# Kernel optimization log

Measured on AMD Instinct MI355X. Metric: run time of the kernel, lower is better.

Reference implementation:

```python
import jax, jax.numpy as jnp
import numpy as np


def setup_inputs() -> dict:
    key = jax.random.key(0)
    kq, kk, kv = jax.random.split(key, 3)
    shape = (4, 16, 2048, 128)  # [B, H, S, D]
    return {
        "query": jax.random.normal(kq, shape, dtype=jnp.float32),
        "key": jax.random.normal(kk, shape, dtype=jnp.float32),
        "value": jax.random.normal(kv, shape, dtype=jnp.float32),
    }


def reference(query, key, value):
    # NOTE: the original torch code computes math.sqrt(d) but immediately
    # overwrites it with d itself, so the scale is 1/D (not 1/sqrt(D)).
    d = query.shape[-1]
    score = jnp.einsum("bhqd,bhkd->bhqk", query, key) / d  # [B,H,S,S]
    attn = jax.nn.softmax(score, axis=-1)
    return jnp.einsum("bhqk,bhkd->bhqd", attn, value)
```

## Files before the change

### kernel.cpp

```cpp
#include <hip/hip_runtime.h>
#include <stdint.h>

typedef __bf16 bf16x8 __attribute__((ext_vector_type(8)));
typedef __bf16 bf16x2 __attribute__((ext_vector_type(2)));
typedef float  f32x4  __attribute__((ext_vector_type(4)));
typedef unsigned short u16x4 __attribute__((ext_vector_type(4)));
typedef unsigned short u16x8 __attribute__((ext_vector_type(8)));

#define DEVI __device__ __forceinline__

constexpr int Bc = 4, Hc = 16, Ss = 2048, Dd = 128;
constexpr int BH = Bc * Hc;
constexpr int BM = 256;
constexpr int MT = 4;
constexpr int BN = 32;
constexpr int NTIL = Ss / BN;
constexpr int LDP = 40;
constexpr float SCALE = 1.44269504088896340736f / 128.0f;

constexpr int TILE_B = BN * Dd * 2;
constexpr int SK_OFF = 0;
constexpr int SV_OFF = 2 * TILE_B;
constexpr int SP_OFF = 4 * TILE_B;
constexpr int LDS_BYTES = SP_OFF + BM * LDP * 2;
static_assert(LDS_BYTES == 53248, "mt=4 config");

DEVI unsigned short f2bf_bits(float x) {
  unsigned u = __builtin_bit_cast(unsigned, x);
  u += 0x7fffu + ((u >> 16) & 1u);
  return (unsigned short)(u >> 16);
}
DEVI __bf16 f2bf(float x) {
  unsigned short b = f2bf_bits(x);
  return __builtin_bit_cast(__bf16, b);
}

DEVI float exp2_hw(float x) { return __builtin_amdgcn_exp2f(x); }

DEVI void gload_lds16(const void* g, void* l) {
  __builtin_amdgcn_global_load_lds(
      (const __attribute__((address_space(1))) unsigned*)(uintptr_t)g,
      (__attribute__((address_space(3))) unsigned*)(unsigned)(uintptr_t)l,
      16, 0, 0);
}

constexpr int LDT2 = 136;
__global__ void k_prep(const float* __restrict__ kin, __bf16* __restrict__ kout,
                       const float* __restrict__ v, __bf16* __restrict__ vt) {
  __shared__ __align__(16) unsigned short tile[64 * LDT2];
  const int bx = blockIdx.x;
  const int u = threadIdx.x;
  if (bx >= 2048) {
    constexpr int N4 = (BH * Ss * Dd) / 4;
    int i = (bx - 2048) * 256 + u;
    const int stride = 2048 * 256;
    #pragma unroll
    for (int it = 0; it < N4 / (2048 * 256); it++, i += stride) {
      float4 x = ((const float4*)kin)[i];
      ushort4 o;
      o.x = f2bf_bits(x.x); o.y = f2bf_bits(x.y);
      o.z = f2bf_bits(x.z); o.w = f2bf_bits(x.w);
      ((ushort4*)kout)[i] = o;
    }
    return;
  }
  const int bh = bx >> 5;
  const int s0 = (bx & 31) * 64;
  const float4* src = (const float4*)(v + ((size_t)bh * Ss + s0) * Dd);
  #pragma unroll
  for (int i = 0; i < 8; i++) {
    int f = i * 256 + u;
    int row = f >> 5;
    int c4 = (f & 31) << 2;
    float4 x = src[f];
    u16x4 o;
    o[0] = f2bf_bits(x.x); o[1] = f2bf_bits(x.y);
    o[2] = f2bf_bits(x.z); o[3] = f2bf_bits(x.w);
    *(u16x4*)&tile[row * LDT2 + c4] = o;
  }
  __syncthreads();
  const int so = u & 7;
  const int dq = u >> 3;
  u16x4 tin[8];
  #pragma unroll
  for (int i = 0; i < 8; i++)
    tin[i] = *(const u16x4*)&tile[(so * 8 + i) * LDT2 + dq * 4];
  #pragma unroll
  for (int j = 0; j < 4; j++) {
    u16x8 o;
    #pragma unroll
    for (int i = 0; i < 8; i++) o[i] = tin[i][j];
    *(u16x8*)(vt + ((size_t)bh * Dd + dq * 4 + j) * Ss + s0 + so * 8) = o;
  }
}

__launch_bounds__(256, 2)
__global__ void k_flash(const float* __restrict__ Q, const __bf16* __restrict__ Kb,
                        const __bf16* __restrict__ Vt, float* __restrict__ O) {
  __shared__ __align__(16) char lds[LDS_BYTES];
  unsigned short* sP = (unsigned short*)(lds + SP_OFF);

  const int tid = threadIdx.x;
  const int w = tid >> 6;
  const int lane = tid & 63;
  const int quad = lane >> 4;
  const int l16 = lane & 15;

  const int bx = blockIdx.x;
  const int bh = bx & (BH - 1);
  const int q0 = (bx >> 6) * BM;

  bf16x8 qa[MT][4];
  {
    const float* qb = Q + ((size_t)bh * Ss + q0 + w * 64) * Dd;
    #pragma unroll
    for (int mt = 0; mt < MT; mt++)
      #pragma unroll
      for (int kk = 0; kk < 4; kk++) {
        const float* p = qb + (mt * 16 + l16) * Dd + kk * 32 + quad * 8;
        float4 a = ((const float4*)p)[0];
        float4 b = ((const float4*)p)[1];
        bf16x8 f;
        f[0] = f2bf(a.x * SCALE); f[1] = f2bf(a.y * SCALE);
        f[2] = f2bf(a.z * SCALE); f[3] = f2bf(a.w * SCALE);
        f[4] = f2bf(b.x * SCALE); f[5] = f2bf(b.y * SCALE);
        f[6] = f2bf(b.z * SCALE); f[7] = f2bf(b.w * SCALE);
        qa[mt][kk] = f;
      }
  }

  f32x4 acc[MT][8];
  #pragma unroll
  for (int mt = 0; mt < MT; mt++)
    #pragma unroll
    for (int dt = 0; dt < 8; dt++)
      acc[mt][dt] = (f32x4){0.f, 0.f, 0.f, 0.f};

  float lacc[MT] = {0.f, 0.f, 0.f, 0.f};

  const __bf16* kbh = Kb + (size_t)bh * Ss * Dd;
  const __bf16* vbh = Vt + (size_t)bh * Ss * Dd;

  const char* gp[4];
  unsigned lo[4];
  int ginc;
  if (w < 2) {
    #pragma unroll
    for (int i = 0; i < 4; i++) {
      const int fk = w * 4 + i, kk = fk >> 1, nt = fk & 1;
      gp[i] = (const char*)(kbh + (size_t)(nt * 16 + l16) * Dd + kk * 32 + quad * 8);
      lo[i] = (unsigned)(SK_OFF + fk * 1024 + lane * 16);
    }
    ginc = BN * Dd * 2;
  } else {
    #pragma unroll
    for (int i = 0; i < 4; i++) {
      const int dt = (w - 2) * 4 + i;
      gp[i] = (const char*)(vbh + (size_t)(dt * 16 + l16) * Ss + quad * 8);
      lo[i] = (unsigned)(SV_OFF + dt * 1024 + lane * 16);
    }
    ginc = BN * 2;
  }

  #pragma unroll
  for (int i = 0; i < 4; i++) gload_lds16(gp[i], lds + lo[i]);
  #pragma unroll
  for (int i = 0; i < 4; i++) gp[i] += ginc;
  __syncthreads();

  unsigned cur = 0;
  for (int t = 0; t < NTIL; t++) {
    if (t < NTIL - 1) {
      const unsigned nb = (cur ^ 1u) * (unsigned)TILE_B;
      #pragma unroll
      for (int i = 0; i < 4; i++) gload_lds16(gp[i], lds + lo[i] + nb);
      #pragma unroll
      for (int i = 0; i < 4; i++) gp[i] += ginc;
    }
    const char* bK = lds + SK_OFF + cur * TILE_B;
    const char* bV = lds + SV_OFF + cur * TILE_B;

    #pragma unroll
    for (int nt = 0; nt < 2; nt++) {
      f32x4 sc[MT];
      #pragma unroll
      for (int mt = 0; mt < MT; mt++) sc[mt] = (f32x4){0.f, 0.f, 0.f, 0.f};
      __builtin_amdgcn_s_setprio(1);
      #pragma unroll
      for (int kk = 0; kk < 4; kk++) {
        bf16x8 bk = *(const bf16x8*)(bK + (kk * 2 + nt) * 1024 + lane * 16);
        #pragma unroll
        for (int mt = 0; mt < MT; mt++)
          sc[mt] = __builtin_amdgcn_mfma_f32_16x16x32_bf16(bk, qa[mt][kk], sc[mt], 0, 0, 0);
      }
      __builtin_amdgcn_s_setprio(0);
      #pragma unroll
      for (int mt = 0; mt < MT; mt++) {
        float p0 = exp2_hw(sc[mt][0]);
        float p1 = exp2_hw(sc[mt][1]);
        float p2 = exp2_hw(sc[mt][2]);
        float p3 = exp2_hw(sc[mt][3]);
        lacc[mt] += (p0 + p1) + (p2 + p3);
        bf16x2 ba, bb;
        ba[0] = (__bf16)p0; ba[1] = (__bf16)p1;
        bb[0] = (__bf16)p2; bb[1] = (__bf16)p3;
        uint2 pw;
        pw.x = __builtin_bit_cast(unsigned, ba);
        pw.y = __builtin_bit_cast(unsigned, bb);
        *(uint2*)(sP + (w * 64 + mt * 16 + l16) * LDP + nt * 16 + quad * 4) = pw;
      }
    }

    bf16x8 pa[MT];
    #pragma unroll
    for (int mt = 0; mt < MT; mt++)
      pa[mt] = *(const bf16x8*)((const char*)sP +
               (size_t)((w * 64 + mt * 16 + l16) * LDP + quad * 8) * 2);
    __builtin_amdgcn_s_setprio(1);
    #pragma unroll
    for (int dt = 0; dt < 8; dt++) {
      bf16x8 bv = *(const bf16x8*)(bV + dt * 1024 + lane * 16);
      #pragma unroll
      for (int mt = 0; mt < MT; mt++)
        acc[mt][dt] = __builtin_amdgcn_mfma_f32_16x16x32_bf16(pa[mt], bv, acc[mt][dt], 0, 0, 0);
    }
    __builtin_amdgcn_s_setprio(0);

    __syncthreads();
    cur ^= 1u;
  }

  float inv_l[MT][4];
  #pragma unroll
  for (int mt = 0; mt < MT; mt++) {
    float l = lacc[mt];
    l += __shfl_xor(l, 16);
    l += __shfl_xor(l, 32);
    #pragma unroll
    for (int r = 0; r < 4; r++) {
      float lr = __shfl(l, (lane & 48) | (quad * 4 + r));
      inv_l[mt][r] = 1.0f / lr;
    }
  }

  float* ob = O + ((size_t)bh * Ss + q0 + w * 64) * Dd;
  #pragma unroll
  for (int mt = 0; mt < MT; mt++)
    #pragma unroll
    for (int r = 0; r < 4; r++) {
      const float inv = inv_l[mt][r];
      const int row = mt * 16 + quad * 4 + r;
      #pragma unroll
      for (int dt = 0; dt < 8; dt++)
        ob[row * Dd + dt * 16 + l16] = acc[mt][dt][r] * inv;
    }
}

extern "C" void kernel_launch(void* const* d_in, const int* in_sizes, int n_in,
                              void* d_out, int out_size, void* d_ws, size_t ws_size,
                              hipStream_t stream) {
  const float* Q = (const float*)d_in[0];
  const float* K = (const float*)d_in[1];
  const float* V = (const float*)d_in[2];
  float* O = (float*)d_out;
  const size_t elems = (size_t)BH * Ss * Dd;
  __bf16* Kb = (__bf16*)d_ws;
  __bf16* Vt = Kb + elems;

  k_prep<<<4096, 256, 0, stream>>>(K, Kb, V, Vt);
  k_flash<<<dim3((Ss / BM) * BH), 256, 0, stream>>>(Q, Kb, Vt, O);
}
```

Baseline: 346.9 us.

## Software-pipeline QK^T of next tile with PV of previous tile in flash loop

Restructures the attention main loop so each iteration computes the QK^T scores and exp for tile t+1 while issuing the PV MFMAs for tile t. The score/exp work and the PV matrix multiplies are interleaved to hide exp and LDS latency, with a prologue computing the first tile's P and an epilogue doing the last PV. K is now prefetched two tiles ahead and V one tile ahead in the double buffers. The setprio hints are removed. This brings more complex buffer indexing and a sync ordering that must hold when P in LDS is overwritten while the previous P is still held in registers.

```diff
diff --git a/kernel.cpp b/kernel.cpp
--- a/kernel.cpp
+++ b/kernel.cpp
@@ -162,30 +162,24 @@
     ginc = BN * 2;
   }
 
-  #pragma unroll
-  for (int i = 0; i < 4; i++) gload_lds16(gp[i], lds + lo[i]);
-  #pragma unroll
-  for (int i = 0; i < 4; i++) gp[i] += ginc;
+  if (w < 2) {
+    #pragma unroll
+    for (int i = 0; i < 4; i++) { gload_lds16(gp[i], lds + lo[i]); gp[i] += ginc; }
+    #pragma unroll
+    for (int i = 0; i < 4; i++) { gload_lds16(gp[i], lds + lo[i] + TILE_B); gp[i] += ginc; }
+  } else {
+    #pragma unroll
+    for (int i = 0; i < 4; i++) { gload_lds16(gp[i], lds + lo[i]); gp[i] += ginc; }
+  }
   __syncthreads();
 
-  unsigned cur = 0;
-  for (int t = 0; t < NTIL; t++) {
-    if (t < NTIL - 1) {
-      const unsigned nb = (cur ^ 1u) * (unsigned)TILE_B;
-      #pragma unroll
-      for (int i = 0; i < 4; i++) gload_lds16(gp[i], lds + lo[i] + nb);
-      #pragma unroll
-      for (int i = 0; i < 4; i++) gp[i] += ginc;
-    }
-    const char* bK = lds + SK_OFF + cur * TILE_B;
-    const char* bV = lds + SV_OFF + cur * TILE_B;
-
+  {
+    const char* bK = lds + SK_OFF;
     #pragma unroll
     for (int nt = 0; nt < 2; nt++) {
       f32x4 sc[MT];
       #pragma unroll
       for (int mt = 0; mt < MT; mt++) sc[mt] = (f32x4){0.f, 0.f, 0.f, 0.f};
-      __builtin_amdgcn_s_setprio(1);
       #pragma unroll
       for (int kk = 0; kk < 4; kk++) {
         bf16x8 bk = *(const bf16x8*)(bK + (kk * 2 + nt) * 1024 + lane * 16);
@@ -193,7 +187,6 @@
         for (int mt = 0; mt < MT; mt++)
           sc[mt] = __builtin_amdgcn_mfma_f32_16x16x32_bf16(bk, qa[mt][kk], sc[mt], 0, 0, 0);
       }
-      __builtin_amdgcn_s_setprio(0);
       #pragma unroll
       for (int mt = 0; mt < MT; mt++) {
         float p0 = exp2_hw(sc[mt][0]);
@@ -210,13 +203,78 @@
         *(uint2*)(sP + (w * 64 + mt * 16 + l16) * LDP + nt * 16 + quad * 4) = pw;
       }
     }
+  }
+  __syncthreads();
+
+  for (int t = 0; t < NTIL - 1; t++) {
+    const unsigned kst = (unsigned)(t & 1) * (unsigned)TILE_B;
+    if (w < 2) {
+      if (t < NTIL - 2) {
+        #pragma unroll
+        for (int i = 0; i < 4; i++) { gload_lds16(gp[i], lds + lo[i] + kst); gp[i] += ginc; }
+      }
+    } else {
+      #pragma unroll
+      for (int i = 0; i < 4; i++) {
+        gload_lds16(gp[i], lds + lo[i] + (kst ^ (unsigned)TILE_B)); gp[i] += ginc;
+      }
+    }
+    const char* bK = lds + SK_OFF + (kst ^ (unsigned)TILE_B);
+    const char* bV = lds + SV_OFF + kst;
 
     bf16x8 pa[MT];
     #pragma unroll
     for (int mt = 0; mt < MT; mt++)
       pa[mt] = *(const bf16x8*)((const char*)sP +
                (size_t)((w * 64 + mt * 16 + l16) * LDP + quad * 8) * 2);
-    __builtin_amdgcn_s_setprio(1);
+
+    #pragma unroll
+    for (int half = 0; half < 2; half++) {
+      const int nt = half;
+      f32x4 sc[MT];
+      #pragma unroll
+      for (int mt = 0; mt < MT; mt++) sc[mt] = (f32x4){0.f, 0.f, 0.f, 0.f};
+      #pragma unroll
+      for (int kk = 0; kk < 4; kk++) {
+        bf16x8 bk = *(const bf16x8*)(bK + (kk * 2 + nt) * 1024 + lane * 16);
+        #pragma unroll
+        for (int mt = 0; mt < MT; mt++)
+          sc[mt] = __builtin_amdgcn_mfma_f32_16x16x32_bf16(bk, qa[mt][kk], sc[mt], 0, 0, 0);
+      }
+      #pragma unroll
+      for (int dt = half * 4; dt < half * 4 + 4; dt++) {
+        bf16x8 bv = *(const bf16x8*)(bV + dt * 1024 + lane * 16);
+        #pragma unroll
+        for (int mt = 0; mt < MT; mt++)
+          acc[mt][dt] = __builtin_amdgcn_mfma_f32_16x16x32_bf16(pa[mt], bv, acc[mt][dt], 0, 0, 0);
+      }
+      #pragma unroll
+      for (int mt = 0; mt < MT; mt++) {
+        float p0 = exp2_hw(sc[mt][0]);
+        float p1 = exp2_hw(sc[mt][1]);
+        float p2 = exp2_hw(sc[mt][2]);
+        float p3 = exp2_hw(sc[mt][3]);
+        lacc[mt] += (p0 + p1) + (p2 + p3);
+        bf16x2 ba, bb;
+        ba[0] = (__bf16)p0; ba[1] = (__bf16)p1;
+        bb[0] = (__bf16)p2; bb[1] = (__bf16)p3;
+        uint2 pw;
+        pw.x = __builtin_bit_cast(unsigned, ba);
+        pw.y = __builtin_bit_cast(unsigned, bb);
+        *(uint2*)(sP + (w * 64 + mt * 16 + l16) * LDP + nt * 16 + quad * 4) = pw;
+      }
+    }
+
+    __syncthreads();
+  }
+
+  {
+    const char* bV = lds + SV_OFF + TILE_B;
+    bf16x8 pa[MT];
+    #pragma unroll
+    for (int mt = 0; mt < MT; mt++)
+      pa[mt] = *(const bf16x8*)((const char*)sP +
+               (size_t)((w * 64 + mt * 16 + l16) * LDP + quad * 8) * 2);
     #pragma unroll
     for (int dt = 0; dt < 8; dt++) {
       bf16x8 bv = *(const bf16x8*)(bV + dt * 1024 + lane * 16);
@@ -224,10 +282,6 @@
       for (int mt = 0; mt < MT; mt++)
         acc[mt][dt] = __builtin_amdgcn_mfma_f32_16x16x32_bf16(pa[mt], bv, acc[mt][dt], 0, 0, 0);
     }
-    __builtin_amdgcn_s_setprio(0);
-
-    __syncthreads();
-    cur ^= 1u;
   }
 
   float inv_l[MT][4];
```

Measured after the change: 411.9 us. 18.8% more time.

## Keep P in registers by permuting K row order to match MFMA operand layout

Applied to the files above, without the earlier changes.

Loads K rows in a permuted order within each 32-key tile so that the score MFMA output layout lines up directly with the A-operand layout needed by the PV MFMA. The P tile now stays in registers instead of taking an LDS write/read round trip, and the LDS P buffer is removed, shrinking shared memory. The cost is a gather-style key ordering on global loads. The result is only correct if the permutation exactly matches the V key order for each lane.

```diff
diff --git a/kernel.cpp b/kernel.cpp
--- a/kernel.cpp
+++ b/kernel.cpp
@@ -15,15 +15,12 @@
 constexpr int MT = 4;
 constexpr int BN = 32;
 constexpr int NTIL = Ss / BN;
-constexpr int LDP = 40;
 constexpr float SCALE = 1.44269504088896340736f / 128.0f;
 
 constexpr int TILE_B = BN * Dd * 2;
 constexpr int SK_OFF = 0;
 constexpr int SV_OFF = 2 * TILE_B;
-constexpr int SP_OFF = 4 * TILE_B;
-constexpr int LDS_BYTES = SP_OFF + BM * LDP * 2;
-static_assert(LDS_BYTES == 53248, "mt=4 config");
+constexpr int LDS_BYTES = 4 * TILE_B;
 
 DEVI unsigned short f2bf_bits(float x) {
   unsigned u = __builtin_bit_cast(unsigned, x);
@@ -33,6 +30,10 @@
 DEVI __bf16 f2bf(float x) {
   unsigned short b = f2bf_bits(x);
   return __builtin_bit_cast(__bf16, b);
+}
+DEVI unsigned pk2(float a, float b) {
+  bf16x2 t; t[0] = (__bf16)a; t[1] = (__bf16)b;
+  return __builtin_bit_cast(unsigned, t);
 }
 
 DEVI float exp2_hw(float x) { return __builtin_amdgcn_exp2f(x); }
@@ -98,7 +99,6 @@
 __global__ void k_flash(const float* __restrict__ Q, const __bf16* __restrict__ Kb,
                         const __bf16* __restrict__ Vt, float* __restrict__ O) {
   __shared__ __align__(16) char lds[LDS_BYTES];
-  unsigned short* sP = (unsigned short*)(lds + SP_OFF);
 
   const int tid = threadIdx.x;
   const int w = tid >> 6;
@@ -148,7 +148,8 @@
     #pragma unroll
     for (int i = 0; i < 4; i++) {
       const int fk = w * 4 + i, kk = fk >> 1, nt = fk & 1;
-      gp[i] = (const char*)(kbh + (size_t)(nt * 16 + l16) * Dd + kk * 32 + quad * 8);
+      const int key = 8 * (l16 >> 2) + 4 * nt + (l16 & 3);
+      gp[i] = (const char*)(kbh + (size_t)key * Dd + kk * 32 + quad * 8);
       lo[i] = (unsigned)(SK_OFF + fk * 1024 + lane * 16);
     }
     ginc = BN * Dd * 2;
@@ -180,6 +181,7 @@
     const char* bK = lds + SK_OFF + cur * TILE_B;
     const char* bV = lds + SV_OFF + cur * TILE_B;
 
+    unsigned pp[MT][4];
     #pragma unroll
     for (int nt = 0; nt < 2; nt++) {
       f32x4 sc[MT];
@@ -201,21 +203,17 @@
         float p2 = exp2_hw(sc[mt][2]);
         float p3 = exp2_hw(sc[mt][3]);
         lacc[mt] += (p0 + p1) + (p2 + p3);
-        bf16x2 ba, bb;
-        ba[0] = (__bf16)p0; ba[1] = (__bf16)p1;
-        bb[0] = (__bf16)p2; bb[1] = (__bf16)p3;
-        uint2 pw;
-        pw.x = __builtin_bit_cast(unsigned, ba);
-        pw.y = __builtin_bit_cast(unsigned, bb);
-        *(uint2*)(sP + (w * 64 + mt * 16 + l16) * LDP + nt * 16 + quad * 4) = pw;
+        pp[mt][nt * 2 + 0] = pk2(p0, p1);
+        pp[mt][nt * 2 + 1] = pk2(p2, p3);
       }
     }
 
     bf16x8 pa[MT];
     #pragma unroll
-    for (int mt = 0; mt < MT; mt++)
-      pa[mt] = *(const bf16x8*)((const char*)sP +
-               (size_t)((w * 64 + mt * 16 + l16) * LDP + quad * 8) * 2);
+    for (int mt = 0; mt < MT; mt++) {
+      uint4 u4 = make_uint4(pp[mt][0], pp[mt][1], pp[mt][2], pp[mt][3]);
+      pa[mt] = __builtin_bit_cast(bf16x8, u4);
+    }
     __builtin_amdgcn_s_setprio(1);
     #pragma unroll
     for (int dt = 0; dt < 8; dt++) {
```

Result: no change. 349.0 us (+0.6%).
